# Kernel optimization log

Hardware: AMD Instinct MI355X
Metric: run time of the kernel (lower is better)

The kernel has to match this reference:

```python
import jax, jax.numpy as jnp
import numpy as np

N_ITEMS = 100000
N_EDGES = 800000
D = 64
N_LAYERS = 3  # config['ii_layers']


def setup_inputs() -> dict:
    key = jax.random.key(0)
    k1, k2, k3, k4 = jax.random.split(key, 4)
    rows = jax.random.randint(k1, (N_EDGES,), 0, N_ITEMS, dtype=jnp.int64 if jax.config.jax_enable_x64 else jnp.int32)
    cols = jax.random.randint(k2, (N_EDGES,), 0, N_ITEMS, dtype=jnp.int64 if jax.config.jax_enable_x64 else jnp.int32)
    vals = jax.random.uniform(k3, (N_EDGES,), dtype=jnp.float32)
    item_embeddings = jax.random.normal(k4, (N_ITEMS, D), dtype=jnp.float32)
    return {"rows": rows, "cols": cols, "vals": vals, "item_embeddings": item_embeddings}


def _spmm(rows, cols, vals, x):
    # sparse.mm(A, x) with A in COO: out[r] += vals[e] * x[c] for each edge e=(r,c)
    msgs = vals[:, None] * x[cols]            # [E, D] gathered & weighted messages
    return jax.ops.segment_sum(msgs, rows, num_segments=N_ITEMS)


def reference(rows, cols, vals, item_embeddings):
    # HyperConv: iterate SpMM, average initial + all layer outputs (fused running sum).
    acc = item_embeddings
    cur = item_embeddings
    for _ in range(N_LAYERS):
        cur = _spmm(rows, cols, vals, cur)
        acc = acc + cur
    return acc / jnp.asarray(N_LAYERS + 1, dtype=item_embeddings.dtype)
```

## Files before the change

### kernel.cpp

```cpp
#include <hip/hip_runtime.h>
#include <hip/hip_fp16.h>


#define NI 100000
#define NE 800000
#define DD 64

#define RPB  512
#define BINS ((NI + RPB - 1) / RPB)
#define EPB  1024
#define P1B  ((NE + EPB - 1) / EPB)
#define CAP  5120
#define BC   32

__global__ __launch_bounds__(256) void part1_k(const int* __restrict__ rows,
                                               const int* __restrict__ cols,
                                               const float* __restrict__ vals,
                                               int* __restrict__ bin_cnt,
                                               int2* __restrict__ binned) {
    __shared__ int hist[BINS], base[BINS], cur[BINS];
    int t = threadIdx.x;
    for (int i = t; i < BINS; i += 256) hist[i] = 0;
    __syncthreads();
    int e0 = blockIdx.x * EPB;
    for (int i = t; i < EPB; i += 256) {
        int e = e0 + i;
        if (e < NE) atomicAdd(&hist[rows[e] >> 9], 1);
    }
    __syncthreads();
    for (int i = t; i < BINS; i += 256) {
        int c = hist[i];
        base[i] = c ? atomicAdd(&bin_cnt[i], c) : 0;
        cur[i] = 0;
    }
    __syncthreads();
    for (int i = t; i < EPB; i += 256) {
        int e = e0 + i;
        if (e < NE) {
            int r = rows[e];
            int b = r >> 9;
            int pos = base[b] + atomicAdd(&cur[b], 1);
            if (pos < CAP)
                binned[(size_t)b * CAP + pos] =
                    make_int2(((r & 511) << 17) | cols[e], __float_as_int(vals[e]));
        }
    }
}

__global__ __launch_bounds__(256) void part2_k(const int* __restrict__ bin_cnt,
                                               const int2* __restrict__ binned,
                                               int2* __restrict__ bucket,
                                               int* __restrict__ fill) {
    __shared__ int cur[RPB];
    int t = threadIdx.x;
    int b = blockIdx.x;
    for (int i = t; i < RPB; i += 256) cur[i] = 0;
    __syncthreads();
    int cnt = bin_cnt[b];
    if (cnt > CAP) cnt = CAP;
    const int2* src = binned + (size_t)b * CAP;
    for (int i = t; i < cnt; i += 256) {
        int2 e = src[i];
        int rl = e.x >> 17;
        int pos = atomicAdd(&cur[rl], 1);
        if (pos < BC)
            bucket[((size_t)b * RPB + rl) * BC + pos] = make_int2(e.x & 0x1FFFF, e.y);
    }
    __syncthreads();
    for (int i = t; i < RPB; i += 256) {
        int r = b * RPB + i;
        if (r < NI) {
            int c = (cur[i] < BC) ? cur[i] : BC;
            if (c & 1) {
                bucket[((size_t)b * RPB + i) * BC + c] = make_int2(0, 0);
                c++;
            }
            fill[r] = c;
        }
    }
}

__global__ __launch_bounds__(256) void convert_k(const float4* __restrict__ x,
                                                 __half* __restrict__ xh, int n4) {
    int i = blockIdx.x * 256 + threadIdx.x;
    if (i < n4) {
        float4 v = x[i];
        __half2* dst = (__half2*)(xh + (size_t)i * 4);
        dst[0] = __floats2half2_rn(v.x, v.y);
        dst[1] = __floats2half2_rn(v.z, v.w);
    }
}

template <int MODE>
__global__ __launch_bounds__(256) void spmm_k(const int* __restrict__ fill,
                                              const int2* __restrict__ bucket,
                                              const __half* __restrict__ xin,
                                              __half* __restrict__ nxt,
                                              const float* __restrict__ x0,
                                              const __half* __restrict__ s1,
                                              float* __restrict__ outp) {
    int tid  = threadIdx.x;
    int lane = tid & 63;
    int grp  = lane >> 3;
    int ll   = lane & 7;
    int r    = blockIdx.x * 32 + (tid >> 6) * 8 + grp;
    int deg  = fill[r];
    const int2* ep = bucket + (size_t)r * BC;

    int wmax = deg;
    wmax = max(wmax, __shfl_xor(wmax, 8, 64));
    wmax = max(wmax, __shfl_xor(wmax, 16, 64));
    wmax = max(wmax, __shfl_xor(wmax, 32, 64));

    uint4 q0 = *(const uint4*)(ep + 2 * ll);
    uint4 q1 = make_uint4(0u, 0u, 0u, 0u);
    if (wmax > 16) q1 = *(const uint4*)(ep + 16 + 2 * ll);

    float a0 = 0.f, a1 = 0.f, a2 = 0.f, a3 = 0.f;
    float a4 = 0.f, a5 = 0.f, a6 = 0.f, a7 = 0.f;

    for (int j = 0; j < wmax; j += 2) {
        int src = (lane & 56) | ((j >> 1) & 7);
        uint4 q = (j < 16) ? q0 : q1;
        int c0  = __shfl((int)q.x, src, 64);
        int v0i = __shfl((int)q.y, src, 64);
        int c1  = __shfl((int)q.z, src, 64);
        int v1i = __shfl((int)q.w, src, 64);
        if (j < deg) {
            uint4 g0 = *(const uint4*)(xin + (size_t)c0 * DD + 8 * ll);
            uint4 g1 = *(const uint4*)(xin + (size_t)c1 * DD + 8 * ll);
            float v0 = __int_as_float(v0i);
            float v1 = __int_as_float(v1i);
            float2 f;
            f = __half22float2(*(__half2*)&g0.x); a0 += v0 * f.x; a1 += v0 * f.y;
            f = __half22float2(*(__half2*)&g0.y); a2 += v0 * f.x; a3 += v0 * f.y;
            f = __half22float2(*(__half2*)&g0.z); a4 += v0 * f.x; a5 += v0 * f.y;
            f = __half22float2(*(__half2*)&g0.w); a6 += v0 * f.x; a7 += v0 * f.y;
            f = __half22float2(*(__half2*)&g1.x); a0 += v1 * f.x; a1 += v1 * f.y;
            f = __half22float2(*(__half2*)&g1.y); a2 += v1 * f.x; a3 += v1 * f.y;
            f = __half22float2(*(__half2*)&g1.z); a4 += v1 * f.x; a5 += v1 * f.y;
            f = __half22float2(*(__half2*)&g1.w); a6 += v1 * f.x; a7 += v1 * f.y;
        }
    }

    if (MODE == 2) {
        size_t fo = (size_t)r * DD + 8 * ll;
        const float4* xp = (const float4*)(x0 + fo);
        float4 xa = xp[0], xb = xp[1];
        uint4 s1u = *(const uint4*)(s1 + fo);
        uint4 s2u = *(const uint4*)(xin + fo);
        float4 oa, ob;
        float2 f1, f2;
        f1 = __half22float2(*(__half2*)&s1u.x); f2 = __half22float2(*(__half2*)&s2u.x);
        oa.x = (xa.x + f1.x + f2.x + a0) * 0.25f;
        oa.y = (xa.y + f1.y + f2.y + a1) * 0.25f;
        f1 = __half22float2(*(__half2*)&s1u.y); f2 = __half22float2(*(__half2*)&s2u.y);
        oa.z = (xa.z + f1.x + f2.x + a2) * 0.25f;
        oa.w = (xa.w + f1.y + f2.y + a3) * 0.25f;
        f1 = __half22float2(*(__half2*)&s1u.z); f2 = __half22float2(*(__half2*)&s2u.z);
        ob.x = (xb.x + f1.x + f2.x + a4) * 0.25f;
        ob.y = (xb.y + f1.y + f2.y + a5) * 0.25f;
        f1 = __half22float2(*(__half2*)&s1u.w); f2 = __half22float2(*(__half2*)&s2u.w);
        ob.z = (xb.z + f1.x + f2.x + a6) * 0.25f;
        ob.w = (xb.w + f1.y + f2.y + a7) * 0.25f;
        float4* op = (float4*)(outp + fo);
        op[0] = oa;
        op[1] = ob;
    } else {
        uint4 o;
        __half2 h;
        h = __floats2half2_rn(a0, a1); o.x = *(uint*)&h;
        h = __floats2half2_rn(a2, a3); o.y = *(uint*)&h;
        h = __floats2half2_rn(a4, a5); o.z = *(uint*)&h;
        h = __floats2half2_rn(a6, a7); o.w = *(uint*)&h;
        *(uint4*)(nxt + (size_t)r * DD + 8 * ll) = o;
    }
}

#define NB ((NI + 255) / 256)

__global__ __launch_bounds__(256) void init_k(const float4* __restrict__ x,
                                              float4* __restrict__ cur,
                                              float4* __restrict__ acc, int n4) {
    int i = blockIdx.x * 256 + threadIdx.x;
    if (i < n4) { float4 v = x[i]; cur[i] = v; acc[i] = v; }
}

__global__ __launch_bounds__(256) void hist_k(const int* __restrict__ rows,
                                              int* __restrict__ counts) {
    int e = blockIdx.x * 256 + threadIdx.x;
    if (e < NE) atomicAdd(&counts[rows[e]], 1);
}

__global__ __launch_bounds__(256) void scan1_k(const int* __restrict__ counts,
                                               int* __restrict__ bsum) {
    __shared__ int s[256];
    int t = threadIdx.x;
    int i = blockIdx.x * 256 + t;
    s[t] = (i < NI) ? counts[i] : 0;
    __syncthreads();
    for (int off = 128; off > 0; off >>= 1) {
        if (t < off) s[t] += s[t + off];
        __syncthreads();
    }
    if (t == 0) bsum[blockIdx.x] = s[0];
}

__global__ __launch_bounds__(512) void scan2_k(int* __restrict__ bsum) {
    __shared__ int s[512];
    int t = threadIdx.x;
    int v = (t < NB) ? bsum[t] : 0;
    s[t] = v;
    __syncthreads();
    for (int off = 1; off < 512; off <<= 1) {
        int tmp = (t >= off) ? s[t - off] : 0;
        __syncthreads();
        s[t] += tmp;
        __syncthreads();
    }
    if (t < NB) bsum[t] = s[t] - v;
}

__global__ __launch_bounds__(256) void scan3_k(const int* __restrict__ counts,
                                               const int* __restrict__ bsum,
                                               int* __restrict__ rowptr) {
    __shared__ int s[256];
    int t = threadIdx.x;
    int i = blockIdx.x * 256 + t;
    int v = (i < NI) ? counts[i] : 0;
    s[t] = v;
    __syncthreads();
    for (int off = 1; off < 256; off <<= 1) {
        int tmp = (t >= off) ? s[t - off] : 0;
        __syncthreads();
        s[t] += tmp;
        __syncthreads();
    }
    int excl = s[t] - v + bsum[blockIdx.x];
    if (i < NI) rowptr[i] = excl;
    if (i == NI - 1) rowptr[NI] = excl + v;
}

__global__ __launch_bounds__(256) void scatter_k(const int* __restrict__ rows,
                                                 const int* __restrict__ cols,
                                                 const float* __restrict__ vals,
                                                 const int* __restrict__ rowptr,
                                                 int* __restrict__ fillc,
                                                 int2* __restrict__ edges) {
    int e = blockIdx.x * 256 + threadIdx.x;
    if (e < NE) {
        int r = rows[e];
        int pos = rowptr[r] + atomicAdd(&fillc[r], 1);
        edges[pos] = make_int2(cols[e], __float_as_int(vals[e]));
    }
}

__global__ __launch_bounds__(256) void spmm_csr_k(const int* __restrict__ rowptr,
                                                  const int2* __restrict__ edges,
                                                  const float* __restrict__ x,
                                                  float* __restrict__ nxt,
                                                  float* __restrict__ acc,
                                                  int last) {
    int r = __builtin_amdgcn_readfirstlane(blockIdx.x * 4 + (threadIdx.x >> 6));
    int lane = threadIdx.x & 63;
    int beg = rowptr[r];
    int end = rowptr[r + 1];
    float s = 0.f;
    int j = beg;
    for (; j + 3 < end; j += 4) {
        int2 e0 = edges[j], e1 = edges[j + 1], e2 = edges[j + 2], e3 = edges[j + 3];
        float g0 = x[(size_t)e0.x * DD + lane];
        float g1 = x[(size_t)e1.x * DD + lane];
        float g2 = x[(size_t)e2.x * DD + lane];
        float g3 = x[(size_t)e3.x * DD + lane];
        s += __int_as_float(e0.y) * g0; s += __int_as_float(e1.y) * g1;
        s += __int_as_float(e2.y) * g2; s += __int_as_float(e3.y) * g3;
    }
    for (; j < end; ++j) {
        int2 e = edges[j];
        s += __int_as_float(e.y) * x[(size_t)e.x * DD + lane];
    }
    size_t o = (size_t)r * DD + lane;
    if (last) acc[o] = (acc[o] + s) * 0.25f;
    else { nxt[o] = s; acc[o] += s; }
}

extern "C" void kernel_launch(void* const* d_in, const int* in_sizes, int n_in,
                              void* d_out, int out_size, void* d_ws, size_t ws_size,
                              hipStream_t stream) {
    const int*   rows = (const int*)d_in[0];
    const int*   cols = (const int*)d_in[1];
    const float* vals = (const float*)d_in[2];
    const float* x    = (const float*)d_in[3];
    float* outp = (float*)d_out;

    const size_t fbuf  = (size_t)NI * DD * sizeof(float);
    const size_t hbuf  = (size_t)NI * DD * sizeof(__half);
    const int    n4        = NI * DD / 4;
    const int    grid_elem = (n4 + 255) / 256;

    char* wsp = (char*)d_ws;

    size_t off_xh     = 0;
    size_t off_s1     = off_xh + hbuf;
    size_t off_s2     = off_s1 + hbuf;
    size_t off_bucket = off_s2 + hbuf;
    size_t off_binned = off_bucket + (size_t)NI * BC * 8;
    size_t off_fill   = off_binned + (size_t)BINS * CAP * 8;
    size_t off_bcnt   = off_fill + (size_t)NI * 4;
    size_t need       = off_bcnt + (size_t)BINS * 4;

    if (ws_size >= need) {
        __half* xh      = (__half*)(wsp + off_xh);
        __half* s1h     = (__half*)(wsp + off_s1);
        __half* s2h     = (__half*)(wsp + off_s2);
        int2*   bucket  = (int2*)(wsp + off_bucket);
        int2*   binned  = (int2*)(wsp + off_binned);
        int*    fill    = (int*)(wsp + off_fill);
        int*    bin_cnt = (int*)(wsp + off_bcnt);

        hipMemsetAsync(bin_cnt, 0, BINS * sizeof(int), stream);
        part1_k<<<P1B, 256, 0, stream>>>(rows, cols, vals, bin_cnt, binned);
        part2_k<<<BINS, 256, 0, stream>>>(bin_cnt, binned, bucket, fill);
        convert_k<<<grid_elem, 256, 0, stream>>>((const float4*)x, xh, n4);

        const int grid_spmm = NI / 32;
        spmm_k<0><<<grid_spmm, 256, 0, stream>>>(fill, bucket, xh,  s1h, nullptr, nullptr, nullptr);
        spmm_k<1><<<grid_spmm, 256, 0, stream>>>(fill, bucket, s1h, s2h, nullptr, nullptr, nullptr);
        spmm_k<2><<<grid_spmm, 256, 0, stream>>>(fill, bucket, s2h, nullptr, x, s1h, outp);
        return;
    }

    const int grid_edge = (NE + 255) / 256;
    const int grid_csr  = NI / 4;

    float* bufA   = (float*)wsp;
    float* bufB   = (float*)(wsp + fbuf);
    int2*  edges  = (int2*)(wsp + 2 * fbuf);
    int*   rowptr = (int*)(wsp + 2 * fbuf + (size_t)NE * 8);
    int*   counts = rowptr + (NI + 1);
    int*   bsum   = counts + NI;

    hipMemsetAsync(counts, 0, NI * sizeof(int), stream);
    hist_k<<<grid_edge, 256, 0, stream>>>(rows, counts);
    scan1_k<<<NB, 256, 0, stream>>>(counts, bsum);
    scan2_k<<<1, 512, 0, stream>>>(bsum);
    scan3_k<<<NB, 256, 0, stream>>>(counts, bsum, rowptr);
    hipMemsetAsync(counts, 0, NI * sizeof(int), stream);
    scatter_k<<<grid_edge, 256, 0, stream>>>(rows, cols, vals, rowptr, counts, edges);
    init_k<<<grid_elem, 256, 0, stream>>>((const float4*)x, (float4*)bufA,
                                          (float4*)outp, n4);
    spmm_csr_k<<<grid_csr, 256, 0, stream>>>(rowptr, edges, bufA, bufB, outp, 0);
    spmm_csr_k<<<grid_csr, 256, 0, stream>>>(rowptr, edges, bufB, bufA, outp, 0);
    spmm_csr_k<<<grid_csr, 256, 0, stream>>>(rowptr, edges, bufA, bufB, outp, 1);
}
```

Measured before the change: 187.8 us.

## Replace two-pass binned bucketing with direct atomic scatter into per-row buckets

Drops the two-stage bin partitioning (part1/part2 plus a memset) and instead zeroes the per-row fill counters inside the conversion kernel, then scatters each edge directly into its row's fixed-size bucket with global atomics. The SpMM kernel clamps the degree, loads only the valid bucket entries, skips the second gather when an odd tail remains, and uses nontemporal loads and stores for streamed data. This removes one launch and the intermediate binned buffer round trip. In exchange it relies on scattered global atomics and uncoalesced bucket writes, and edge order within a row becomes nondeterministic.

```diff
diff --git a/kernel.cpp b/kernel.cpp
--- a/kernel.cpp
+++ b/kernel.cpp
@@ -5,89 +5,41 @@
 #define NI 100000
 #define NE 800000
 #define DD 64
-
-#define RPB  512
-#define BINS ((NI + RPB - 1) / RPB)
-#define EPB  1024
-#define P1B  ((NE + EPB - 1) / EPB)
-#define CAP  5120
-#define BC   32
-
-__global__ __launch_bounds__(256) void part1_k(const int* __restrict__ rows,
-                                               const int* __restrict__ cols,
-                                               const float* __restrict__ vals,
-                                               int* __restrict__ bin_cnt,
-                                               int2* __restrict__ binned) {
-    __shared__ int hist[BINS], base[BINS], cur[BINS];
-    int t = threadIdx.x;
-    for (int i = t; i < BINS; i += 256) hist[i] = 0;
-    __syncthreads();
-    int e0 = blockIdx.x * EPB;
-    for (int i = t; i < EPB; i += 256) {
-        int e = e0 + i;
-        if (e < NE) atomicAdd(&hist[rows[e] >> 9], 1);
-    }
-    __syncthreads();
-    for (int i = t; i < BINS; i += 256) {
-        int c = hist[i];
-        base[i] = c ? atomicAdd(&bin_cnt[i], c) : 0;
-        cur[i] = 0;
-    }
-    __syncthreads();
-    for (int i = t; i < EPB; i += 256) {
-        int e = e0 + i;
-        if (e < NE) {
-            int r = rows[e];
-            int b = r >> 9;
-            int pos = base[b] + atomicAdd(&cur[b], 1);
-            if (pos < CAP)
-                binned[(size_t)b * CAP + pos] =
-                    make_int2(((r & 511) << 17) | cols[e], __float_as_int(vals[e]));
-        }
-    }
-}
-
-__global__ __launch_bounds__(256) void part2_k(const int* __restrict__ bin_cnt,
-                                               const int2* __restrict__ binned,
-                                               int2* __restrict__ bucket,
-                                               int* __restrict__ fill) {
-    __shared__ int cur[RPB];
-    int t = threadIdx.x;
-    int b = blockIdx.x;
-    for (int i = t; i < RPB; i += 256) cur[i] = 0;
-    __syncthreads();
-    int cnt = bin_cnt[b];
-    if (cnt > CAP) cnt = CAP;
-    const int2* src = binned + (size_t)b * CAP;
-    for (int i = t; i < cnt; i += 256) {
-        int2 e = src[i];
-        int rl = e.x >> 17;
-        int pos = atomicAdd(&cur[rl], 1);
-        if (pos < BC)
-            bucket[((size_t)b * RPB + rl) * BC + pos] = make_int2(e.x & 0x1FFFF, e.y);
-    }
-    __syncthreads();
-    for (int i = t; i < RPB; i += 256) {
-        int r = b * RPB + i;
-        if (r < NI) {
-            int c = (cur[i] < BC) ? cur[i] : BC;
-            if (c & 1) {
-                bucket[((size_t)b * RPB + i) * BC + c] = make_int2(0, 0);
-                c++;
-            }
-            fill[r] = c;
-        }
-    }
-}
-
-__global__ __launch_bounds__(256) void convert_k(const float4* __restrict__ x,
-                                                 __half* __restrict__ xh, int n4) {
+#define BC 32
+
+typedef int   i4 __attribute__((ext_vector_type(4)));
+typedef float f4 __attribute__((ext_vector_type(4)));
+
+static __device__ __forceinline__ float2 h2f(int w) {
+    __half2 h = *(__half2*)&w;
+    return __half22float2(h);
+}
+
+__global__ __launch_bounds__(256) void convert_zero_k(const float4* __restrict__ x,
+                                                      __half* __restrict__ xh,
+                                                      int* __restrict__ fill,
+                                                      int n4) {
     int i = blockIdx.x * 256 + threadIdx.x;
+    if (i < NI) fill[i] = 0;
     if (i < n4) {
         float4 v = x[i];
         __half2* dst = (__half2*)(xh + (size_t)i * 4);
         dst[0] = __floats2half2_rn(v.x, v.y);
         dst[1] = __floats2half2_rn(v.z, v.w);
+    }
+}
+
+__global__ __launch_bounds__(256) void scatter_b_k(const int* __restrict__ rows,
+                                                   const int* __restrict__ cols,
+                                                   const float* __restrict__ vals,
+                                                   int* __restrict__ fill,
+                                                   int2* __restrict__ bucket) {
+    int e = blockIdx.x * 256 + threadIdx.x;
+    if (e < NE) {
+        int r = rows[e];
+        int pos = atomicAdd(&fill[r], 1);
+        if (pos < BC)
+            bucket[(size_t)r * BC + pos] = make_int2(cols[e], __float_as_int(vals[e]));
     }
 }
 
@@ -105,6 +57,7 @@
     int ll   = lane & 7;
     int r    = blockIdx.x * 32 + (tid >> 6) * 8 + grp;
     int deg  = fill[r];
+    if (deg > BC) deg = BC;
     const int2* ep = bucket + (size_t)r * BC;
 
     int wmax = deg;
@@ -112,68 +65,70 @@
     wmax = max(wmax, __shfl_xor(wmax, 16, 64));
     wmax = max(wmax, __shfl_xor(wmax, 32, 64));
 
-    uint4 q0 = *(const uint4*)(ep + 2 * ll);
-    uint4 q1 = make_uint4(0u, 0u, 0u, 0u);
-    if (wmax > 16) q1 = *(const uint4*)(ep + 16 + 2 * ll);
+    i4 q0 = (i4)0, q1 = (i4)0;
+    if (2 * ll < deg)      q0 = __builtin_nontemporal_load((const i4*)(ep + 2 * ll));
+    if (16 + 2 * ll < deg) q1 = __builtin_nontemporal_load((const i4*)(ep + 16 + 2 * ll));
 
     float a0 = 0.f, a1 = 0.f, a2 = 0.f, a3 = 0.f;
     float a4 = 0.f, a5 = 0.f, a6 = 0.f, a7 = 0.f;
 
     for (int j = 0; j < wmax; j += 2) {
         int src = (lane & 56) | ((j >> 1) & 7);
-        uint4 q = (j < 16) ? q0 : q1;
-        int c0  = __shfl((int)q.x, src, 64);
-        int v0i = __shfl((int)q.y, src, 64);
-        int c1  = __shfl((int)q.z, src, 64);
-        int v1i = __shfl((int)q.w, src, 64);
+        i4 q = (j < 16) ? q0 : q1;
+        int c0  = __shfl(q[0], src, 64);
+        int v0i = __shfl(q[1], src, 64);
+        int c1  = __shfl(q[2], src, 64);
+        int v1i = __shfl(q[3], src, 64);
         if (j < deg) {
-            uint4 g0 = *(const uint4*)(xin + (size_t)c0 * DD + 8 * ll);
-            uint4 g1 = *(const uint4*)(xin + (size_t)c1 * DD + 8 * ll);
+            i4 g0 = *(const i4*)(xin + (size_t)c0 * DD + 8 * ll);
             float v0 = __int_as_float(v0i);
-            float v1 = __int_as_float(v1i);
             float2 f;
-            f = __half22float2(*(__half2*)&g0.x); a0 += v0 * f.x; a1 += v0 * f.y;
-            f = __half22float2(*(__half2*)&g0.y); a2 += v0 * f.x; a3 += v0 * f.y;
-            f = __half22float2(*(__half2*)&g0.z); a4 += v0 * f.x; a5 += v0 * f.y;
-            f = __half22float2(*(__half2*)&g0.w); a6 += v0 * f.x; a7 += v0 * f.y;
-            f = __half22float2(*(__half2*)&g1.x); a0 += v1 * f.x; a1 += v1 * f.y;
-            f = __half22float2(*(__half2*)&g1.y); a2 += v1 * f.x; a3 += v1 * f.y;
-            f = __half22float2(*(__half2*)&g1.z); a4 += v1 * f.x; a5 += v1 * f.y;
-            f = __half22float2(*(__half2*)&g1.w); a6 += v1 * f.x; a7 += v1 * f.y;
+            f = h2f(g0[0]); a0 += v0 * f.x; a1 += v0 * f.y;
+            f = h2f(g0[1]); a2 += v0 * f.x; a3 += v0 * f.y;
+            f = h2f(g0[2]); a4 += v0 * f.x; a5 += v0 * f.y;
+            f = h2f(g0[3]); a6 += v0 * f.x; a7 += v0 * f.y;
+            if (j + 1 < deg) {
+                i4 g1 = *(const i4*)(xin + (size_t)c1 * DD + 8 * ll);
+                float v1 = __int_as_float(v1i);
+                f = h2f(g1[0]); a0 += v1 * f.x; a1 += v1 * f.y;
+                f = h2f(g1[1]); a2 += v1 * f.x; a3 += v1 * f.y;
+                f = h2f(g1[2]); a4 += v1 * f.x; a5 += v1 * f.y;
+                f = h2f(g1[3]); a6 += v1 * f.x; a7 += v1 * f.y;
+            }
         }
     }
 
     if (MODE == 2) {
         size_t fo = (size_t)r * DD + 8 * ll;
-        const float4* xp = (const float4*)(x0 + fo);
-        float4 xa = xp[0], xb = xp[1];
-        uint4 s1u = *(const uint4*)(s1 + fo);
-        uint4 s2u = *(const uint4*)(xin + fo);
-        float4 oa, ob;
+        f4 xa = __builtin_nontemporal_load((const f4*)(x0 + fo));
+        f4 xb = __builtin_nontemporal_load((const f4*)(x0 + fo) + 1);
+        i4 s1u = __builtin_nontemporal_load((const i4*)(s1 + fo));
+        i4 s2u = *(const i4*)(xin + fo);
+        f4 oa, ob;
         float2 f1, f2;
-        f1 = __half22float2(*(__half2*)&s1u.x); f2 = __half22float2(*(__half2*)&s2u.x);
-        oa.x = (xa.x + f1.x + f2.x + a0) * 0.25f;
-        oa.y = (xa.y + f1.y + f2.y + a1) * 0.25f;
-        f1 = __half22float2(*(__half2*)&s1u.y); f2 = __half22float2(*(__half2*)&s2u.y);
-        oa.z = (xa.z + f1.x + f2.x + a2) * 0.25f;
-        oa.w = (xa.w + f1.y + f2.y + a3) * 0.25f;
-        f1 = __half22float2(*(__half2*)&s1u.z); f2 = __half22float2(*(__half2*)&s2u.z);
-        ob.x = (xb.x + f1.x + f2.x + a4) * 0.25f;
-        ob.y = (xb.y + f1.y + f2.y + a5) * 0.25f;
-        f1 = __half22float2(*(__half2*)&s1u.w); f2 = __half22float2(*(__half2*)&s2u.w);
-        ob.z = (xb.z + f1.x + f2.x + a6) * 0.25f;
-        ob.w = (xb.w + f1.y + f2.y + a7) * 0.25f;
-        float4* op = (float4*)(outp + fo);
-        op[0] = oa;
-        op[1] = ob;
+        f1 = h2f(s1u[0]); f2 = h2f(s2u[0]);
+        oa[0] = (xa[0] + f1.x + f2.x + a0) * 0.25f;
+        oa[1] = (xa[1] + f1.y + f2.y + a1) * 0.25f;
+        f1 = h2f(s1u[1]); f2 = h2f(s2u[1]);
+        oa[2] = (xa[2] + f1.x + f2.x + a2) * 0.25f;
+        oa[3] = (xa[3] + f1.y + f2.y + a3) * 0.25f;
+        f1 = h2f(s1u[2]); f2 = h2f(s2u[2]);
+        ob[0] = (xb[0] + f1.x + f2.x + a4) * 0.25f;
+        ob[1] = (xb[1] + f1.y + f2.y + a5) * 0.25f;
+        f1 = h2f(s1u[3]); f2 = h2f(s2u[3]);
+        ob[2] = (xb[2] + f1.x + f2.x + a6) * 0.25f;
+        ob[3] = (xb[3] + f1.y + f2.y + a7) * 0.25f;
+        f4* op = (f4*)(outp + fo);
+        __builtin_nontemporal_store(oa, op);
+        __builtin_nontemporal_store(ob, op + 1);
     } else {
-        uint4 o;
+        i4 o;
         __half2 h;
-        h = __floats2half2_rn(a0, a1); o.x = *(uint*)&h;
-        h = __floats2half2_rn(a2, a3); o.y = *(uint*)&h;
-        h = __floats2half2_rn(a4, a5); o.z = *(uint*)&h;
-        h = __floats2half2_rn(a6, a7); o.w = *(uint*)&h;
-        *(uint4*)(nxt + (size_t)r * DD + 8 * ll) = o;
+        h = __floats2half2_rn(a0, a1); o[0] = *(int*)&h;
+        h = __floats2half2_rn(a2, a3); o[1] = *(int*)&h;
+        h = __floats2half2_rn(a4, a5); o[2] = *(int*)&h;
+        h = __floats2half2_rn(a6, a7); o[3] = *(int*)&h;
+        *(i4*)(nxt + (size_t)r * DD + 8 * ll) = o;
     }
 }
 
@@ -305,24 +260,18 @@
     size_t off_s1     = off_xh + hbuf;
     size_t off_s2     = off_s1 + hbuf;
     size_t off_bucket = off_s2 + hbuf;
-    size_t off_binned = off_bucket + (size_t)NI * BC * 8;
-    size_t off_fill   = off_binned + (size_t)BINS * CAP * 8;
-    size_t off_bcnt   = off_fill + (size_t)NI * 4;
-    size_t need       = off_bcnt + (size_t)BINS * 4;
+    size_t off_fill   = off_bucket + (size_t)NI * BC * 8;
+    size_t need       = off_fill + (size_t)NI * 4;
 
     if (ws_size >= need) {
-        __half* xh      = (__half*)(wsp + off_xh);
-        __half* s1h     = (__half*)(wsp + off_s1);
-        __half* s2h     = (__half*)(wsp + off_s2);
-        int2*   bucket  = (int2*)(wsp + off_bucket);
-        int2*   binned  = (int2*)(wsp + off_binned);
-        int*    fill    = (int*)(wsp + off_fill);
-        int*    bin_cnt = (int*)(wsp + off_bcnt);
-
-        hipMemsetAsync(bin_cnt, 0, BINS * sizeof(int), stream);
-        part1_k<<<P1B, 256, 0, stream>>>(rows, cols, vals, bin_cnt, binned);
-        part2_k<<<BINS, 256, 0, stream>>>(bin_cnt, binned, bucket, fill);
-        convert_k<<<grid_elem, 256, 0, stream>>>((const float4*)x, xh, n4);
+        __half* xh     = (__half*)(wsp + off_xh);
+        __half* s1h    = (__half*)(wsp + off_s1);
+        __half* s2h    = (__half*)(wsp + off_s2);
+        int2*   bucket = (int2*)(wsp + off_bucket);
+        int*    fill   = (int*)(wsp + off_fill);
+
+        convert_zero_k<<<grid_elem, 256, 0, stream>>>((const float4*)x, xh, fill, n4);
+        scatter_b_k<<<(NE + 255) / 256, 256, 0, stream>>>(rows, cols, vals, fill, bucket);
 
         const int grid_spmm = NI / 32;
         spmm_k<0><<<grid_spmm, 256, 0, stream>>>(fill, bucket, xh,  s1h, nullptr, nullptr, nullptr);
```

Result: slower. 200.4 us (+6.7%).
